# Kernel tuning notes

Hardware: AMD Instinct MI355X
Metric: run time of the kernel (lower is better)

Reference implementation:

```python
import jax, jax.numpy as jnp
import numpy as np

IN_F, OUT_F, K, STRIDE, PAD = 256, 256, 3, 1, 1
SEARCH_SPACE = (2, 4, 8, 16)  # derived in __init__ from in/out=256, feature_size=16


def _cir_project(weight, b):
    """Circulant projection of conv weight for block size b.
    Equivalent to the nested diagonal-mean + roll loops in trans_to_cir:
      tc[q,p,i] = mean_j tmp[q,p,j,(j+i)%b]   (wrapped diagonal mean)
      w[q,p,r,c] = tc[q,p,(r-c)%b]            (roll construction)
    """
    q, p = OUT_F // b, IN_F // b
    tmp = weight.reshape(q, b, p, b, K, K).transpose(0, 2, 1, 3, 4, 5)  # (q,p,b,b,k,k)
    j = jnp.arange(b)
    diag_idx = (j[:, None] + j[None, :]) % b          # (b_j, b_i)
    tc = tmp[:, :, j[:, None], diag_idx].mean(axis=2)  # (q,p,b,k,k)
    circ_idx = (j[:, None] - j[None, :]) % b          # (r, c)
    w = tc[:, :, circ_idx]                             # (q,p,b,b,k,k)
    return w.transpose(0, 2, 1, 3, 4, 5).reshape(OUT_F, IN_F, K, K)


def setup_inputs() -> dict:
    key = jax.random.key(0)
    k1, k2 = jax.random.split(key, 2)
    x = jax.random.normal(k1, (256, IN_F, 16, 16), jnp.float32)
    weight = jax.random.normal(k2, (OUT_F, IN_F, K, K), jnp.float32) * 0.05
    alphas = jnp.ones((len(SEARCH_SPACE) + 1,), jnp.float32)
    return {"x": x, "weight": weight, "alphas": alphas}


def reference(x, weight, alphas):
    # gumbel_softmax with finetune=False -> plain softmax over alphas
    a = jax.nn.softmax(alphas)
    w = a[0] * weight
    for i, b in enumerate(SEARCH_SPACE):
        w = w + a[i + 1] * _cir_project(weight, b)
    return jax.lax.conv_general_dilated(
        x, w,
        window_strides=(STRIDE, STRIDE),
        padding=[(PAD, PAD), (PAD, PAD)],
        dimension_numbers=("NCHW", "OIHW", "NCHW"),
    )
```

## Files before the change

kernel.cpp:

```cpp
#include <hip/hip_runtime.h>
#include <cstdint>
#include <cstddef>

#define NIMG 256
#define PADW 18
#define XB_IMG (PADW * PADW * 256)
#define W2_ROW 2304

typedef __bf16 bf16x8 __attribute__((ext_vector_type(8)));
typedef float floatx4 __attribute__((ext_vector_type(4)));
typedef float floatvec4 __attribute__((ext_vector_type(4)));

__device__ __forceinline__ unsigned short f2bf(float f) {
    unsigned u = __float_as_uint(f);
    u = (u + 0x7FFFu + ((u >> 16) & 1u)) >> 16;
    return (unsigned short)u;
}

__device__ __forceinline__ void gload_lds16(const void* g, void* l) {
    __builtin_amdgcn_global_load_lds(
        (const __attribute__((address_space(1))) void*)g,
        (__attribute__((address_space(3))) void*)l, 16, 0, 0);
}

__global__ __launch_bounds__(256) void convert_kernel(
        const float* __restrict__ x, unsigned short* __restrict__ xb) {
    __shared__ __align__(16) unsigned short tile2[64][268];
    const int n  = blockIdx.x;
    const int c0 = blockIdx.y * 64;
    const int t  = threadIdx.x;
    const float* xi = x + (size_t)n * 65536;
    unsigned short* xo = xb + (size_t)n * XB_IMG;

    if (blockIdx.y == 0) {
        #pragma unroll
        for (int it = 0; it < 17; ++it) {
            int idx = it * 256 + t;
            int hp = idx >> 6;
            int c4 = (idx & 63) * 4;
            int py, px;
            if (hp < 18)      { py = 0;       px = hp;      }
            else if (hp < 36) { py = 17;      px = hp - 18; }
            else if (hp < 52) { py = hp - 35; px = 0;       }
            else              { py = hp - 51; px = 17;      }
            *(uint2*)&xo[(py * 18 + px) * 256 + c4] = make_uint2(0u, 0u);
        }
    }

    {
        const int p4 = (t & 63) * 4;
        const int ci = t >> 6;
        #pragma unroll
        for (int i = 0; i < 16; ++i) {
            const int c = i * 4 + ci;
            floatvec4 v = *(const floatvec4*)&xi[(c0 + c) * 256 + p4];
            unsigned lo = (unsigned)f2bf(v.x) | ((unsigned)f2bf(v.y) << 16);
            unsigned hi = (unsigned)f2bf(v.z) | ((unsigned)f2bf(v.w) << 16);
            *(uint2*)&tile2[c][p4] = make_uint2(lo, hi);
        }
    }
    __syncthreads();

    #pragma unroll
    for (int it = 0; it < 32; ++it) {
        int idx = it * 256 + t;
        int p   = idx >> 5;
        int cp  = (idx & 31) * 2;
        unsigned lo = tile2[cp][p];
        unsigned hi = tile2[cp + 1][p];
        int py = (p >> 4) + 1, px = (p & 15) + 1;
        *(unsigned int*)&xo[(py * 18 + px) * 256 + c0 + cp] = lo | (hi << 16);
    }
}

__global__ __launch_bounds__(256) void wprep_kernel(
        const float* __restrict__ wt, const float* __restrict__ alphas,
        unsigned short* __restrict__ w2) {
    __shared__ float wlds[16][257];
    const int o16 = blockIdx.x * 16;
    const int pos = blockIdx.y;
    const int t   = threadIdx.x;

    #pragma unroll
    for (int j = 0; j < 16; ++j)
        wlds[j][t] = wt[((o16 + j) * 256 + t) * 9 + pos];

    float a[5];
    {
        float mx = alphas[0];
        #pragma unroll
        for (int i = 1; i < 5; ++i) mx = fmaxf(mx, alphas[i]);
        float s = 0.f;
        #pragma unroll
        for (int i = 0; i < 5; ++i) { a[i] = __expf(alphas[i] - mx); s += a[i]; }
        float inv = 1.f / s;
        #pragma unroll
        for (int i = 0; i < 5; ++i) a[i] *= inv;
    }
    __syncthreads();

    const int c = t;
    #pragma unroll
    for (int oo = 0; oo < 16; ++oo) {
        float acc = a[0] * wlds[oo][c];
        #pragma unroll
        for (int bi = 0; bi < 4; ++bi) {
            const int b  = 2 << bi;
            const int r  = oo & (b - 1);
            const int cc = c & (b - 1);
            const int i0 = (r - cc) & (b - 1);
            const int ob = oo - r;
            const int icb = c - cc;
            float s2 = 0.f;
            for (int j = 0; j < b; ++j)
                s2 += wlds[ob + j][icb + ((j + i0) & (b - 1))];
            acc += a[1 + bi] * s2 * (1.f / (float)b);
        }
        w2[(size_t)(o16 + oo) * W2_ROW + pos * 256 + c] = f2bf(acc);
    }
}

struct GemmCtx {
    const unsigned short* xb;
    const unsigned short* w2;
    int xg[8], wg[8];
    int wid, lds_base;
    int arow, brow, sa0, sb0;
};

__device__ __forceinline__ void issue_step(const GemmCtx& c, int st,
                                           unsigned short* XS,
                                           unsigned short* WS) {
    const int pos = st >> 2, cs = st & 3;
    if (c.wid < 2) {
        const int dy = pos / 3, dx = pos - dy * 3;
        const int go = (dy - 1) * (18 * 256) + (dx - 1) * 256 + cs * 64;
        #pragma unroll
        for (int i = 0; i < 8; ++i)
            gload_lds16(c.xb + c.xg[i] + go, &XS[c.lds_base + i * 512]);
    } else {
        const int go = pos * 256 + cs * 64;
        #pragma unroll
        for (int i = 0; i < 8; ++i)
            gload_lds16(c.w2 + c.wg[i] + go, &WS[c.lds_base + i * 512]);
    }
}

__device__ __forceinline__ void compute_step(const GemmCtx& c,
                                             const unsigned short* XS,
                                             const unsigned short* WS,
                                             floatx4 (&acc)[4][4]) {
    #pragma unroll
    for (int ks = 0; ks < 2; ++ks) {
        const int sa = (c.sa0 + ks * 4) & 7;
        const int sb = (c.sb0 + ks * 4) & 7;
        bf16x8 af[4], bfr[4];
        #pragma unroll
        for (int mt = 0; mt < 4; ++mt)
            af[mt] = *(const bf16x8*)&WS[(c.arow + mt * 16) * 64 + sa * 8];
        #pragma unroll
        for (int nt = 0; nt < 4; ++nt)
            bfr[nt] = *(const bf16x8*)&XS[(c.brow + nt * 16) * 64 + sb * 8];
        #pragma unroll
        for (int mt = 0; mt < 4; ++mt)
            #pragma unroll
            for (int nt = 0; nt < 4; ++nt)
                acc[mt][nt] = __builtin_amdgcn_mfma_f32_16x16x32_bf16(
                    af[mt], bfr[nt], acc[mt][nt], 0, 0, 0);
    }
}

__global__ __launch_bounds__(256) void gemm_kernel(
        const unsigned short* __restrict__ xb,
        const unsigned short* __restrict__ w2,
        float* __restrict__ out) {
    __shared__ __align__(16) unsigned short xs0[8192];
    __shared__ __align__(16) unsigned short ws0[8192];
    __shared__ __align__(16) unsigned short xs1[8192];
    __shared__ __align__(16) unsigned short ws1[8192];

    const int t    = threadIdx.x;
    const int lane = t & 63;
    const int wid  = t >> 6;

    const int b     = blockIdx.x;
    const int s_    = b >> 3;
    const int ptile = (b & 7) * 64 + (s_ >> 1);
    const int ktile = s_ & 1;
    const int n_img = ptile >> 1;
    const int half  = ptile & 1;
    const int kbase = ktile * 128;

    GemmCtx c;
    c.xb = xb; c.w2 = w2; c.wid = wid;
    c.lds_base = (wid & 1) * 4096;

    {
        const int rlo  = lane >> 3;
        const int cswz = ((lane & 7) - rlo) & 7;
        const int coff = cswz * 8;
        const int sub  = wid & 1;
        #pragma unroll
        for (int i = 0; i < 8; ++i) {
            int r = sub * 64 + i * 8 + rlo;
            int y  = half * 8 + (r >> 4);
            int xq = r & 15;
            c.xg[i] = n_img * XB_IMG + ((y + 1) * 18 + (xq + 1)) * 256 + coff;
            int kr = kbase + sub * 64 + i * 8 + rlo;
            c.wg[i] = kr * W2_ROW + coff;
        }
    }

    const int wrow = wid >> 1, wcol = wid & 1;
    c.arow = wrow * 64 + (lane & 15);
    c.brow = wcol * 64 + (lane & 15);
    c.sa0  = (c.arow + (lane >> 4)) & 7;
    c.sb0  = (c.brow + (lane >> 4)) & 7;

    const floatx4 z4 = {0.f, 0.f, 0.f, 0.f};
    floatx4 acc[4][4];
    #pragma unroll
    for (int i = 0; i < 4; ++i)
        #pragma unroll
        for (int j = 0; j < 4; ++j) acc[i][j] = z4;

    issue_step(c, 0, xs0, ws0);
    for (int ds2 = 0; ds2 < 18; ++ds2) {
        const int st = ds2 * 2;
        __syncthreads();
        issue_step(c, st + 1, xs1, ws1);
        compute_step(c, xs0, ws0, acc);

        __syncthreads();
        if (ds2 < 17) issue_step(c, st + 2, xs0, ws0);
        compute_step(c, xs1, ws1, acc);
    }

    const int p0 = half * 128 + wcol * 64;
    const int k0 = kbase + wrow * 64;
    float* ob = out + (size_t)n_img * 65536;
    #pragma unroll
    for (int mt = 0; mt < 4; ++mt) {
        #pragma unroll
        for (int nt = 0; nt < 4; ++nt) {
            const int kout = k0 + mt * 16 + (lane >> 4) * 4;
            const int p    = p0 + nt * 16 + (lane & 15);
            #pragma unroll
            for (int r = 0; r < 4; ++r)
                ob[(kout + r) * 256 + p] = acc[mt][nt][r];
        }
    }
}

__global__ __launch_bounds__(256) void naive_conv(
        const float* __restrict__ x, const unsigned short* __restrict__ w2,
        float* __restrict__ out) {
    __shared__ float wr[2304];
    const int n = blockIdx.x >> 8, k = blockIdx.x & 255;
    const int t = threadIdx.x;
    for (int i = t; i < 2304; i += 256)
        wr[i] = __uint_as_float(((unsigned)w2[k * W2_ROW + i]) << 16);
    __syncthreads();
    const int y = t >> 4, xx = t & 15;
    const float* xi = x + (size_t)n * 65536;
    float acc = 0.f;
    for (int pos = 0; pos < 9; ++pos) {
        int dy = pos / 3 - 1, dx = pos % 3 - 1;
        int yy = y + dy, x2 = xx + dx;
        if (yy < 0 || yy > 15 || x2 < 0 || x2 > 15) continue;
        const float* xp = xi + yy * 16 + x2;
        const float* wp = wr + pos * 256;
        for (int c = 0; c < 256; ++c) acc += xp[c * 256] * wp[c];
    }
    out[(size_t)n * 65536 + k * 256 + t] = acc;
}

extern "C" void kernel_launch(void* const* d_in, const int* in_sizes, int n_in,
                              void* d_out, int out_size, void* d_ws, size_t ws_size,
                              hipStream_t stream) {
    const float* x      = (const float*)d_in[0];
    const float* wt     = (const float*)d_in[1];
    const float* alphas = (const float*)d_in[2];
    float* out = (float*)d_out;

    const size_t xb_elems = (size_t)NIMG * XB_IMG;
    const size_t w2_elems = (size_t)256 * W2_ROW;
    const size_t need = (xb_elems + w2_elems) * sizeof(unsigned short);

    if (ws_size >= need) {
        unsigned short* xb = (unsigned short*)d_ws;
        unsigned short* w2 = xb + xb_elems;
        convert_kernel<<<dim3(256, 4), 256, 0, stream>>>(x, xb);
        wprep_kernel<<<dim3(16, 9), 256, 0, stream>>>(wt, alphas, w2);
        gemm_kernel<<<dim3(1024), 256, 0, stream>>>(xb, w2, out);
    } else if (ws_size >= w2_elems * sizeof(unsigned short)) {
        unsigned short* w2 = (unsigned short*)d_ws;
        wprep_kernel<<<dim3(16, 9), 256, 0, stream>>>(wt, alphas, w2);
        naive_conv<<<dim3(256 * 256), 256, 0, stream>>>(x, w2, out);
    }
}
```

Measured before the change: 204.0 us.

## Merge prep kernels and use 4-stage pipelined per-image GEMM with 512 threads

```diff
diff --git a/kernel.cpp b/kernel.cpp
--- a/kernel.cpp
+++ b/kernel.cpp
@@ -23,53 +23,104 @@
         (__attribute__((address_space(3))) void*)l, 16, 0, 0);
 }
 
-__global__ __launch_bounds__(256) void convert_kernel(
-        const float* __restrict__ x, unsigned short* __restrict__ xb) {
-    __shared__ __align__(16) unsigned short tile2[64][268];
-    const int n  = blockIdx.x;
-    const int c0 = blockIdx.y * 64;
+#define VMCNT_LGKM0(n) asm volatile("s_waitcnt vmcnt(" #n ") lgkmcnt(0)" ::: "memory")
+
+__global__ __launch_bounds__(256) void prep_kernel(
+        const float* __restrict__ x, unsigned short* __restrict__ xb,
+        const float* __restrict__ wt, const float* __restrict__ alphas,
+        unsigned short* __restrict__ w2) {
+    __shared__ __align__(16) char lds_pool[64 * 268 * 2];
+    const int bx = blockIdx.x;
     const int t  = threadIdx.x;
-    const float* xi = x + (size_t)n * 65536;
-    unsigned short* xo = xb + (size_t)n * XB_IMG;
-
-    if (blockIdx.y == 0) {
-        #pragma unroll
-        for (int it = 0; it < 17; ++it) {
+
+    if (bx < 1024) {
+        unsigned short (*tile2)[268] = (unsigned short (*)[268])lds_pool;
+        const int n  = bx & 255;
+        const int cy = bx >> 8;
+        const int c0 = cy * 64;
+        const float* xi = x + (size_t)n * 65536;
+        unsigned short* xo = xb + (size_t)n * XB_IMG;
+
+        if (cy == 0) {
+            #pragma unroll
+            for (int it = 0; it < 17; ++it) {
+                int idx = it * 256 + t;
+                int hp = idx >> 6;
+                int c4 = (idx & 63) * 4;
+                int py, px;
+                if (hp < 18)      { py = 0;       px = hp;      }
+                else if (hp < 36) { py = 17;      px = hp - 18; }
+                else if (hp < 52) { py = hp - 35; px = 0;       }
+                else              { py = hp - 51; px = 17;      }
+                *(uint2*)&xo[(py * 18 + px) * 256 + c4] = make_uint2(0u, 0u);
+            }
+        }
+        {
+            const int p4 = (t & 63) * 4;
+            const int ci = t >> 6;
+            #pragma unroll
+            for (int i = 0; i < 16; ++i) {
+                const int c = i * 4 + ci;
+                floatvec4 v = *(const floatvec4*)&xi[(c0 + c) * 256 + p4];
+                unsigned lo = (unsigned)f2bf(v.x) | ((unsigned)f2bf(v.y) << 16);
+                unsigned hi = (unsigned)f2bf(v.z) | ((unsigned)f2bf(v.w) << 16);
+                *(uint2*)&tile2[c][p4] = make_uint2(lo, hi);
+            }
+        }
+        __syncthreads();
+        #pragma unroll
+        for (int it = 0; it < 32; ++it) {
             int idx = it * 256 + t;
-            int hp = idx >> 6;
-            int c4 = (idx & 63) * 4;
-            int py, px;
-            if (hp < 18)      { py = 0;       px = hp;      }
-            else if (hp < 36) { py = 17;      px = hp - 18; }
-            else if (hp < 52) { py = hp - 35; px = 0;       }
-            else              { py = hp - 51; px = 17;      }
-            *(uint2*)&xo[(py * 18 + px) * 256 + c4] = make_uint2(0u, 0u);
-        }
-    }
-
-    {
-        const int p4 = (t & 63) * 4;
-        const int ci = t >> 6;
-        #pragma unroll
-        for (int i = 0; i < 16; ++i) {
-            const int c = i * 4 + ci;
-            floatvec4 v = *(const floatvec4*)&xi[(c0 + c) * 256 + p4];
-            unsigned lo = (unsigned)f2bf(v.x) | ((unsigned)f2bf(v.y) << 16);
-            unsigned hi = (unsigned)f2bf(v.z) | ((unsigned)f2bf(v.w) << 16);
-            *(uint2*)&tile2[c][p4] = make_uint2(lo, hi);
-        }
-    }
-    __syncthreads();
-
-    #pragma unroll
-    for (int it = 0; it < 32; ++it) {
-        int idx = it * 256 + t;
-        int p   = idx >> 5;
-        int cp  = (idx & 31) * 2;
-        unsigned lo = tile2[cp][p];
-        unsigned hi = tile2[cp + 1][p];
-        int py = (p >> 4) + 1, px = (p & 15) + 1;
-        *(unsigned int*)&xo[(py * 18 + px) * 256 + c0 + cp] = lo | (hi << 16);
+            int p   = idx >> 5;
+            int cp  = (idx & 31) * 2;
+            unsigned lo = tile2[cp][p];
+            unsigned hi = tile2[cp + 1][p];
+            int py = (p >> 4) + 1, px = (p & 15) + 1;
+            *(unsigned int*)&xo[(py * 18 + px) * 256 + c0 + cp] = lo | (hi << 16);
+        }
+    } else {
+        float (*wlds)[257] = (float (*)[257])lds_pool;
+        const int w   = bx - 1024;
+        const int o16 = (w & 15) * 16;
+        const int pos = w >> 4;
+
+        #pragma unroll
+        for (int j = 0; j < 16; ++j)
+            wlds[j][t] = wt[((o16 + j) * 256 + t) * 9 + pos];
+
+        float a[5];
+        {
+            float mx = alphas[0];
+            #pragma unroll
+            for (int i = 1; i < 5; ++i) mx = fmaxf(mx, alphas[i]);
+            float s = 0.f;
+            #pragma unroll
+            for (int i = 0; i < 5; ++i) { a[i] = __expf(alphas[i] - mx); s += a[i]; }
+            float inv = 1.f / s;
+            #pragma unroll
+            for (int i = 0; i < 5; ++i) a[i] *= inv;
+        }
+        __syncthreads();
+
+        const int c = t;
+        #pragma unroll
+        for (int oo = 0; oo < 16; ++oo) {
+            float acc = a[0] * wlds[oo][c];
+            #pragma unroll
+            for (int bi = 0; bi < 4; ++bi) {
+                const int b  = 2 << bi;
+                const int r  = oo & (b - 1);
+                const int cc = c & (b - 1);
+                const int i0 = (r - cc) & (b - 1);
+                const int ob = oo - r;
+                const int icb = c - cc;
+                float s2 = 0.f;
+                for (int j = 0; j < b; ++j)
+                    s2 += wlds[ob + j][icb + ((j + i0) & (b - 1))];
+                acc += a[1 + bi] * s2 * (1.f / (float)b);
+            }
+            w2[(size_t)(o16 + oo) * W2_ROW + pos * 256 + c] = f2bf(acc);
+        }
     }
 }
 
@@ -80,11 +131,9 @@
     const int o16 = blockIdx.x * 16;
     const int pos = blockIdx.y;
     const int t   = threadIdx.x;
-
     #pragma unroll
     for (int j = 0; j < 16; ++j)
         wlds[j][t] = wt[((o16 + j) * 256 + t) * 9 + pos];
-
     float a[5];
     {
         float mx = alphas[0];
@@ -98,7 +147,6 @@
         for (int i = 0; i < 5; ++i) a[i] *= inv;
     }
     __syncthreads();
-
     const int c = t;
     #pragma unroll
     for (int oo = 0; oo < 16; ++oo) {
@@ -120,136 +168,147 @@
     }
 }
 
-struct GemmCtx {
-    const unsigned short* xb;
-    const unsigned short* w2;
-    int xg[8], wg[8];
-    int wid, lds_base;
-    int arow, brow, sa0, sb0;
-};
-
-__device__ __forceinline__ void issue_step(const GemmCtx& c, int st,
-                                           unsigned short* XS,
-                                           unsigned short* WS) {
-    const int pos = st >> 2, cs = st & 3;
-    if (c.wid < 2) {
-        const int dy = pos / 3, dx = pos - dy * 3;
-        const int go = (dy - 1) * (18 * 256) + (dx - 1) * 256 + cs * 64;
-        #pragma unroll
-        for (int i = 0; i < 8; ++i)
-            gload_lds16(c.xb + c.xg[i] + go, &XS[c.lds_base + i * 512]);
+__global__ __launch_bounds__(512, 2) void gemm_kernel(
+        const unsigned short* __restrict__ xb,
+        const unsigned short* __restrict__ w2,
+        float* __restrict__ out) {
+    extern __shared__ __align__(16) char smem[];
+    unsigned short* const xs = (unsigned short*)smem;
+    unsigned short* const ws = (unsigned short*)(smem + 65536);
+
+    const int t     = threadIdx.x;
+    const int lane  = t & 63;
+    const int wid   = t >> 6;
+    const int n_img = blockIdx.x;
+
+    const int q     = lane >> 2;
+    const int kswz  = ((lane & 3) - ((lane >> 3) & 3)) & 3;
+    const int choff = kswz * 8;
+    const unsigned short* sbase;
+    int sg[4];
+    int ldst;
+    if (wid < 4) {
+        sbase = xb;
+        #pragma unroll
+        for (int i = 0; i < 4; ++i) {
+            const int r = wid * 64 + i * 16 + q;
+            const int y = r >> 4, xx = r & 15;
+            sg[i] = n_img * XB_IMG + ((y + 1) * 18 + (xx + 1)) * 256 + choff;
+        }
+        ldst = wid * 4096;
     } else {
-        const int go = pos * 256 + cs * 64;
-        #pragma unroll
-        for (int i = 0; i < 8; ++i)
-            gload_lds16(c.w2 + c.wg[i] + go, &WS[c.lds_base + i * 512]);
-    }
-}
-
-__device__ __forceinline__ void compute_step(const GemmCtx& c,
-                                             const unsigned short* XS,
-                                             const unsigned short* WS,
-                                             floatx4 (&acc)[4][4]) {
+        sbase = w2;
+        const int wv = wid - 4;
+        #pragma unroll
+        for (int i = 0; i < 4; ++i) {
+            const int r = wv * 64 + i * 16 + q;
+            sg[i] = r * W2_ROW + choff;
+        }
+        ldst = (wid - 4) * 4096;
+    }
+    const bool is_x = (wid < 4);
+
+    auto issue = [&](int hs, unsigned short* XSb, unsigned short* WSb) {
+        const int pos = hs >> 3, k32 = hs & 7;
+        int go; char* dst;
+        if (is_x) {
+            const int dy = pos / 3, dx = pos - dy * 3;
+            go  = (dy - 1) * 4608 + (dx - 1) * 256 + k32 * 32;
+            dst = (char*)XSb + ldst;
+        } else {
+            go  = pos * 256 + k32 * 32;
+            dst = (char*)WSb + ldst;
+        }
+        #pragma unroll
+        for (int i = 0; i < 4; ++i)
+            gload_lds16(sbase + sg[i] + go, dst + i * 1024);
+    };
+
+    const int wr   = wid >> 2, wc = wid & 3;
+    const int slot = ((lane >> 1) + (lane >> 4)) & 3;
+    const int aoff = (wr * 128 + (lane & 15)) * 32 + slot * 8;
+    const int boff = (wc * 64  + (lane & 15)) * 32 + slot * 8;
+
+    const floatx4 z4 = {0.f, 0.f, 0.f, 0.f};
+    floatx4 acc[8][4];
     #pragma unroll
-    for (int ks = 0; ks < 2; ++ks) {
-        const int sa = (c.sa0 + ks * 4) & 7;
-        const int sb = (c.sb0 + ks * 4) & 7;
-        bf16x8 af[4], bfr[4];
-        #pragma unroll
-        for (int mt = 0; mt < 4; ++mt)
-            af[mt] = *(const bf16x8*)&WS[(c.arow + mt * 16) * 64 + sa * 8];
+    for (int i = 0; i < 8; ++i)
+        #pragma unroll
+        for (int j = 0; j < 4; ++j) acc[i][j] = z4;
+
+    auto compute = [&](const unsigned short* XSb, const unsigned short* WSb) {
+        bf16x8 af[8], bfr[4];
+        #pragma unroll
+        for (int mt = 0; mt < 8; ++mt)
+            af[mt] = *(const bf16x8*)&WSb[aoff + mt * 512];
         #pragma unroll
         for (int nt = 0; nt < 4; ++nt)
-            bfr[nt] = *(const bf16x8*)&XS[(c.brow + nt * 16) * 64 + sb * 8];
-        #pragma unroll
-        for (int mt = 0; mt < 4; ++mt)
+            bfr[nt] = *(const bf16x8*)&XSb[boff + nt * 512];
+        __builtin_amdgcn_s_setprio(1);
+        #pragma unroll
+        for (int mt = 0; mt < 8; ++mt)
             #pragma unroll
             for (int nt = 0; nt < 4; ++nt)
                 acc[mt][nt] = __builtin_amdgcn_mfma_f32_16x16x32_bf16(
                     af[mt], bfr[nt], acc[mt][nt], 0, 0, 0);
-    }
-}
-
-__global__ __launch_bounds__(256) void gemm_kernel(
-        const unsigned short* __restrict__ xb,
-        const unsigned short* __restrict__ w2,
-        float* __restrict__ out) {
-    __shared__ __align__(16) unsigned short xs0[8192];
-    __shared__ __align__(16) unsigned short ws0[8192];
-    __shared__ __align__(16) unsigned short xs1[8192];
-    __shared__ __align__(16) unsigned short ws1[8192];
-
-    const int t    = threadIdx.x;
-    const int lane = t & 63;
-    const int wid  = t >> 6;
-
-    const int b     = blockIdx.x;
-    const int s_    = b >> 3;
-    const int ptile = (b & 7) * 64 + (s_ >> 1);
-    const int ktile = s_ & 1;
-    const int n_img = ptile >> 1;
-    const int half  = ptile & 1;
-    const int kbase = ktile * 128;
-
-    GemmCtx c;
-    c.xb = xb; c.w2 = w2; c.wid = wid;
-    c.lds_base = (wid & 1) * 4096;
-
-    {
-        const int rlo  = lane >> 3;
-        const int cswz = ((lane & 7) - rlo) & 7;
-        const int coff = cswz * 8;
-        const int sub  = wid & 1;
-        #pragma unroll
-        for (int i = 0; i < 8; ++i) {
-            int r = sub * 64 + i * 8 + rlo;
-            int y  = half * 8 + (r >> 4);
-            int xq = r & 15;
-            c.xg[i] = n_img * XB_IMG + ((y + 1) * 18 + (xq + 1)) * 256 + coff;
-            int kr = kbase + sub * 64 + i * 8 + rlo;
-            c.wg[i] = kr * W2_ROW + coff;
-        }
-    }
-
-    const int wrow = wid >> 1, wcol = wid & 1;
-    c.arow = wrow * 64 + (lane & 15);
-    c.brow = wcol * 64 + (lane & 15);
-    c.sa0  = (c.arow + (lane >> 4)) & 7;
-    c.sb0  = (c.brow + (lane >> 4)) & 7;
-
-    const floatx4 z4 = {0.f, 0.f, 0.f, 0.f};
-    floatx4 acc[4][4];
+        __builtin_amdgcn_s_setprio(0);
+    };
+
+    unsigned short* const xs0 = xs,         * const ws0 = ws;
+    unsigned short* const xs1 = xs + 8192,  * const ws1 = ws + 8192;
+    unsigned short* const xs2 = xs + 16384, * const ws2 = ws + 16384;
+    unsigned short* const xs3 = xs + 24576, * const ws3 = ws + 24576;
+
+    issue(0, xs0, ws0);
+    issue(1, xs1, ws1);
+    issue(2, xs2, ws2);
+
+    int hs = 0;
+    #pragma unroll 1
+    for (int it = 0; it < 17; ++it) {
+        VMCNT_LGKM0(8); __builtin_amdgcn_s_barrier();
+        issue(hs + 3, xs3, ws3);
+        compute(xs0, ws0);
+
+        VMCNT_LGKM0(8); __builtin_amdgcn_s_barrier();
+        issue(hs + 4, xs0, ws0);
+        compute(xs1, ws1);
+
+        VMCNT_LGKM0(8); __builtin_amdgcn_s_barrier();
+        issue(hs + 5, xs1, ws1);
+        compute(xs2, ws2);
+
+        VMCNT_LGKM0(8); __builtin_amdgcn_s_barrier();
+        issue(hs + 6, xs2, ws2);
+        compute(xs3, ws3);
+        hs += 4;
+    }
+    VMCNT_LGKM0(8); __builtin_amdgcn_s_barrier();
+    issue(71, xs3, ws3);
+    compute(xs0, ws0);
+
+    VMCNT_LGKM0(8); __builtin_amdgcn_s_barrier();
+    compute(xs1, ws1);
+
+    VMCNT_LGKM0(4); __builtin_amdgcn_s_barrier();
+    compute(xs2, ws2);
+
+    VMCNT_LGKM0(0); __builtin_amdgcn_s_barrier();
+    compute(xs3, ws3);
+
+    float* ob = out + (size_t)n_img * 65536;
+    const int kb = wr * 128 + (lane >> 4) * 4;
+    const int pb = wc * 64 + (lane & 15);
     #pragma unroll
-    for (int i = 0; i < 4; ++i)
-        #pragma unroll
-        for (int j = 0; j < 4; ++j) acc[i][j] = z4;
-
-    issue_step(c, 0, xs0, ws0);
-    for (int ds2 = 0; ds2 < 18; ++ds2) {
-        const int st = ds2 * 2;
-        __syncthreads();
-        issue_step(c, st + 1, xs1, ws1);
-        compute_step(c, xs0, ws0, acc);
-
-        __syncthreads();
-        if (ds2 < 17) issue_step(c, st + 2, xs0, ws0);
-        compute_step(c, xs1, ws1, acc);
-    }
-
-    const int p0 = half * 128 + wcol * 64;
-    const int k0 = kbase + wrow * 64;
-    float* ob = out + (size_t)n_img * 65536;
-    #pragma unroll
-    for (int mt = 0; mt < 4; ++mt) {
+    for (int mt = 0; mt < 8; ++mt)
         #pragma unroll
         for (int nt = 0; nt < 4; ++nt) {
-            const int kout = k0 + mt * 16 + (lane >> 4) * 4;
-            const int p    = p0 + nt * 16 + (lane & 15);
+            const int kout = kb + mt * 16;
+            const int p    = pb + nt * 16;
             #pragma unroll
             for (int r = 0; r < 4; ++r)
-                ob[(kout + r) * 256 + p] = acc[mt][nt][r];
-        }
-    }
+                ob[(size_t)(kout + r) * 256 + p] = acc[mt][nt][r];
+        }
 }
 
 __global__ __launch_bounds__(256) void naive_conv(
@@ -288,14 +347,20 @@
     const size_t need = (xb_elems + w2_elems) * sizeof(unsigned short);
 
     if (ws_size >= need) {
-        unsigned short* xb = (unsigned short*)d_ws;
-        unsigned short* w2 = xb + xb_elems;
-        convert_kernel<<<dim3(256, 4), 256, 0, stream>>>(x, xb);
-        wprep_kernel<<<dim3(16, 9), 256, 0, stream>>>(wt, alphas, w2);
-        gemm_kernel<<<dim3(1024), 256, 0, stream>>>(xb, w2, out);
+        unsigned short* xbp = (unsigned short*)d_ws;
+        unsigned short* w2p = xbp + xb_elems;
+        static bool attr_done = false;
+        if (!attr_done) {
+            (void)hipFuncSetAttribute(reinterpret_cast<const void*>(&gemm_kernel),
+                                      hipFuncAttributeMaxDynamicSharedMemorySize,
+                                      131072);
+            attr_done = true;
+        }
+        prep_kernel<<<dim3(1168), 256, 0, stream>>>(x, xbp, wt, alphas, w2p);
+        gemm_kernel<<<dim3(256), 512, 131072, stream>>>(xbp, w2p, out);
     } else if (ws_size >= w2_elems * sizeof(unsigned short)) {
-        unsigned short* w2 = (unsigned short*)d_ws;
-        wprep_kernel<<<dim3(16, 9), 256, 0, stream>>>(wt, alphas, w2);
-        naive_conv<<<dim3(256 * 256), 256, 0, stream>>>(x, w2, out);
-    }
-}
+        unsigned short* w2p = (unsigned short*)d_ws;
+        wprep_kernel<<<dim3(16, 9), 256, 0, stream>>>(wt, alphas, w2p);
+        naive_conv<<<dim3(256 * 256), 256, 0, stream>>>(x, w2p, out);
+    }
+}
```

Measured after the change: 186.9 us. 1.09x faster.
